# Kernel optimization log

Hardware: AMD Instinct MI355X
Metric: run time of the kernel (lower is better)

## Reference

```python
import jax, jax.numpy as jnp
import numpy as np

WH, WW = 7, 7
DIM, HEADS = 256, 8


def make_table_index(wh, ww):
    # relative coords table (log-spaced CPB input) and relative position index
    ch = np.arange(-(wh - 1), wh, dtype=np.float32)
    cw = np.arange(-(ww - 1), ww, dtype=np.float32)
    t = np.stack(np.meshgrid(ch, cw, indexing='ij'), axis=-1)[None]  # [1,2wh-1,2ww-1,2]
    t = t.copy()
    t[..., 0] /= (wh - 1)
    t[..., 1] /= (ww - 1)
    t *= 8.0
    t = np.sign(t) * np.log2(np.abs(t) + 1.0) / np.log2(8.0)
    coords = np.stack(np.meshgrid(np.arange(wh), np.arange(ww), indexing='ij'))
    cf = coords.reshape(2, -1)
    rc = (cf[:, :, None] - cf[:, None, :]).transpose(1, 2, 0).copy()  # [N,N,2]
    rc[..., 0] += wh - 1
    rc[..., 1] += ww - 1
    rc[..., 0] *= 2 * ww - 1
    idx = rc.sum(-1)
    return t.astype(np.float32), idx.astype(np.int32)


def setup_inputs() -> dict:
    key = jax.random.key(0)
    ks = jax.random.split(key, 10)
    B_, N, C, H = 2048, WH * WW, DIM, HEADS
    table, idx = make_table_index(WH, WW)
    return {
        'x': jax.random.normal(ks[0], (B_, N, C), jnp.float32),
        'mask': jnp.zeros((64, N, N), jnp.float32),
        'qkv_w': jax.random.normal(ks[1], (3 * C, C), jnp.float32) * 0.02,
        'q_bias': jnp.zeros((C,), jnp.float32),
        'v_bias': jnp.zeros((C,), jnp.float32),
        'logit_scale': jnp.full((H, 1, 1), np.log(10.0), jnp.float32),
        'cpb_w1': jax.random.normal(ks[2], (512, 2), jnp.float32) * 0.02,
        'cpb_b1': jnp.zeros((512,), jnp.float32),
        'cpb_w2': jax.random.normal(ks[3], (H, 512), jnp.float32) * 0.02,
        'proj_w': jax.random.normal(ks[4], (C, C), jnp.float32) * 0.02,
        'proj_b': jnp.zeros((C,), jnp.float32),
        'rel_coords_table': jnp.asarray(table),
        'rel_pos_index': jnp.asarray(idx),
    }


def _l2norm(t):
    return t / jnp.maximum(jnp.linalg.norm(t, axis=-1, keepdims=True), 1e-12)


def reference(x, mask, qkv_w, q_bias, v_bias, logit_scale, cpb_w1, cpb_b1,
              cpb_w2, proj_w, proj_b, rel_coords_table, rel_pos_index):
    B_, N, C = x.shape
    H = logit_scale.shape[0]
    hd = C // H
    qkv_b = jnp.concatenate([q_bias, jnp.zeros_like(v_bias), v_bias])
    qkv = (x @ qkv_w.T + qkv_b).reshape(B_, N, 3, H, hd).transpose(2, 0, 3, 1, 4)
    q, k, v = qkv[0], qkv[1], qkv[2]  # [B_,H,N,hd]
    attn = jnp.einsum('bhnd,bhmd->bhnm', _l2norm(q), _l2norm(k))
    scale = jnp.exp(jnp.minimum(logit_scale, jnp.log(jnp.float32(100.0))))  # [H,1,1]
    attn = attn * scale[None]
    # CPB MLP -> relative position bias
    table = jax.nn.relu(rel_coords_table @ cpb_w1.T + cpb_b1) @ cpb_w2.T  # [1,Th,Tw,H]
    table = table.reshape(-1, H)
    bias = table[rel_pos_index.reshape(-1)].reshape(N, N, H).transpose(2, 0, 1)
    attn = attn + 16.0 * jax.nn.sigmoid(bias)[None]
    nW = mask.shape[0]
    attn = attn.reshape(B_ // nW, nW, H, N, N) + mask[None, :, None]
    attn = jax.nn.softmax(attn.reshape(B_, H, N, N), axis=-1)
    out = jnp.einsum('bhnm,bhmd->bhnd', attn, v).transpose(0, 2, 1, 3).reshape(B_, N, C)
    return out @ proj_w.T + proj_b
```

## Files before the change

### kernel.cpp

```cpp
#include <hip/hip_runtime.h>

#define DEV __device__ __forceinline__

typedef float  f32x4  __attribute__((ext_vector_type(4)));
typedef __bf16 bf16x8 __attribute__((ext_vector_type(8)));

DEV unsigned short f2bf(float f) {
  unsigned u = __float_as_uint(f);
  u += 0x7fffu + ((u >> 16) & 1u);
  return (unsigned short)(u >> 16);
}
DEV float bf2f(unsigned short v) { return __uint_as_float(((unsigned)v) << 16); }

DEV void cp16(const void* g, void* l) {
  __builtin_amdgcn_global_load_lds((const __attribute__((address_space(1))) void*)g,
                                   (__attribute__((address_space(3))) void*)l, 16, 0, 0);
}

__global__ __launch_bounds__(256) void prep_kernel(
    const float* __restrict__ qkv_w, const float* __restrict__ proj_w,
    const float* __restrict__ q_bias, const float* __restrict__ v_bias,
    unsigned short* __restrict__ wq, unsigned short* __restrict__ wp,
    float* __restrict__ qkvb)
{
  int gid = blockIdx.x * 256 + threadIdx.x;
  if (gid < 196608) wq[gid] = f2bf(qkv_w[gid]);
  else              wp[gid - 196608] = f2bf(proj_w[gid - 196608]);
  if (gid < 768)
    qkvb[gid] = (gid < 256) ? q_bias[gid] : ((gid < 512) ? 0.f : v_bias[gid - 512]);
}

__global__ __launch_bounds__(256) void xcvt(const float* __restrict__ x,
                                            unsigned short* __restrict__ xb)
{
  const size_t g = ((size_t)blockIdx.x * 256 + threadIdx.x) * 8;
  float4 a = *(const float4*)(x + g);
  float4 b = *(const float4*)(x + g + 4);
  uint4 u;
  u.x = f2bf(a.x) | ((unsigned)f2bf(a.y) << 16);
  u.y = f2bf(a.z) | ((unsigned)f2bf(a.w) << 16);
  u.z = f2bf(b.x) | ((unsigned)f2bf(b.y) << 16);
  u.w = f2bf(b.z) | ((unsigned)f2bf(b.w) << 16);
  *(uint4*)(xb + g) = u;
}

__global__ __launch_bounds__(64) void cpb_mlp(
    const float* __restrict__ tab, const float* __restrict__ w1,
    const float* __restrict__ b1, const float* __restrict__ w2,
    float* __restrict__ table16)
{
  int r = blockIdx.x;
  int t = threadIdx.x;
  float x0 = tab[r * 2 + 0], x1 = tab[r * 2 + 1];
  float part[8];
#pragma unroll
  for (int h = 0; h < 8; ++h) part[h] = 0.f;
  for (int j = t; j < 512; j += 64) {
    float hv = fmaxf(w1[j * 2 + 0] * x0 + w1[j * 2 + 1] * x1 + b1[j], 0.f);
#pragma unroll
    for (int h = 0; h < 8; ++h) part[h] += hv * w2[h * 512 + j];
  }
#pragma unroll
  for (int h = 0; h < 8; ++h) {
    float v = part[h];
    for (int off = 32; off > 0; off >>= 1) v += __shfl_down(v, off, 64);
    if (t == 0) table16[r * 8 + h] = 16.f / (1.f + expf(-v));
  }
}

__global__ __launch_bounds__(256) void bmb(
    const float* __restrict__ t16, const int* __restrict__ ridx,
    const float* __restrict__ mask, float* __restrict__ bias64,
    float* __restrict__ mask64)
{
  int gid = blockIdx.x * 256 + threadIdx.x;
  int p = gid & 4095, i = p >> 6, j = p & 63;
  bool valid = (i < 49) && (j < 49);
  if (gid < 32768) {
    int h = gid >> 12;
    bias64[gid] = valid ? t16[ridx[i * 49 + j] * 8 + h] : 0.f;
  } else {
    int g2 = gid - 32768;
    int w = g2 >> 12;
    mask64[g2] = valid ? mask[w * 2401 + i * 49 + j] : 0.f;
  }
}

template <bool OBF16>
__global__ __launch_bounds__(256) void gemm128(
    const unsigned short* __restrict__ A, const unsigned short* __restrict__ W,
    const float* __restrict__ bias, void* __restrict__ Yp, int N, int K)
{
  __shared__ __align__(1024) unsigned short sA[128 * 64];
  __shared__ __align__(1024) unsigned short sB[128 * 64];
  const int t = threadIdx.x, w = t >> 6, l = t & 63, quad = l >> 4, l15 = l & 15;
  const int bm = blockIdx.y * 128, bn = blockIdx.x * 128;
  const int wm = (w >> 1) * 64, wn = (w & 1) * 64;
  const int srow = t >> 3, sch = t & 7;

  f32x4 acc[4][4] = {};
  const int KT = K >> 6;
  for (int kt = 0; kt < KT; ++kt) {
    const int k0 = kt << 6;
    if (kt) __syncthreads();
#pragma unroll
    for (int i = 0; i < 4; ++i) {
      const int row = i * 32 + srow;
      const int sc  = sch ^ (srow & 7);
      cp16(A + (size_t)(bm + row) * K + k0 + sc * 8, sA + (i * 256 + w * 64) * 8);
      cp16(W + (size_t)(bn + row) * K + k0 + sc * 8, sB + (i * 256 + w * 64) * 8);
    }
    __syncthreads();
#pragma unroll
    for (int kk = 0; kk < 2; ++kk) {
      bf16x8 af[4], bfr[4];
#pragma unroll
      for (int mt = 0; mt < 4; ++mt)
        af[mt] = *(const bf16x8*)&sA[(wm + mt * 16 + l15) * 64 + (((4 * kk + quad) ^ (l15 & 7)) * 8)];
#pragma unroll
      for (int nt = 0; nt < 4; ++nt)
        bfr[nt] = *(const bf16x8*)&sB[(wn + nt * 16 + l15) * 64 + (((4 * kk + quad) ^ (l15 & 7)) * 8)];
#pragma unroll
      for (int mt = 0; mt < 4; ++mt)
#pragma unroll
        for (int nt = 0; nt < 4; ++nt)
          acc[mt][nt] = __builtin_amdgcn_mfma_f32_16x16x32_bf16(af[mt], bfr[nt], acc[mt][nt], 0, 0, 0);
    }
  }
#pragma unroll
  for (int nt = 0; nt < 4; ++nt) {
    const int col = bn + wn + nt * 16 + l15;
    const float bv = bias[col];
#pragma unroll
    for (int mt = 0; mt < 4; ++mt) {
#pragma unroll
      for (int r = 0; r < 4; ++r) {
        const int row = bm + wm + mt * 16 + quad * 4 + r;
        float v = acc[mt][nt][r] + bv;
        if constexpr (OBF16) ((unsigned short*)Yp)[(size_t)row * N + col] = f2bf(v);
        else                 ((float*)Yp)[(size_t)row * N + col] = v;
      }
    }
  }
}

__global__ __launch_bounds__(256) void attn_mfma(
    const unsigned short* __restrict__ qkv, const float* __restrict__ logit_scale,
    const float* __restrict__ bias64, const float* __restrict__ mask64,
    unsigned short* __restrict__ aout)
{
  __shared__ __align__(1024) char smem[4 * 12800];
  const int w = threadIdx.x >> 6, l = threadIdx.x & 63, quad = l >> 4, l15 = l & 15;
  const int flat = blockIdx.x * 4 + w;
  const int b = flat >> 3, h = flat & 7;
  char* my = smem + w * 12800;
  unsigned short* vT = (unsigned short*)my;
  unsigned short* P  = (unsigned short*)(my + 4096);
  float* rq = (float*)(my + 12288);
  float* rk = (float*)(my + 12544);

  const size_t base = (size_t)b * 49 * 768 + h * 32;

  if (l < 49) {
    const unsigned short* qp = qkv + base + (size_t)l * 768;
    unsigned short qb_[32], kb_[32], vb_[32];
#pragma unroll
    for (int c = 0; c < 4; ++c) {
      *(uint4*)&qb_[c * 8] = *(const uint4*)(qp + c * 8);
      *(uint4*)&kb_[c * 8] = *(const uint4*)(qp + 256 + c * 8);
      *(uint4*)&vb_[c * 8] = *(const uint4*)(qp + 512 + c * 8);
    }
    float sq = 0.f, sk = 0.f;
#pragma unroll
    for (int d = 0; d < 32; ++d) {
      float qf = bf2f(qb_[d]), kf = bf2f(kb_[d]);
      sq += qf * qf; sk += kf * kf;
    }
    const float scale = __expf(fminf(logit_scale[h], 4.60517019f));
    rq[l] = scale / fmaxf(sqrtf(sq), 1e-12f);
    rk[l] = 1.f / fmaxf(sqrtf(sk), 1e-12f);
#pragma unroll
    for (int d = 0; d < 32; ++d)
      vT[d * 64 + (((l >> 3) ^ (d & 7)) << 3) + (l & 7)] = vb_[d];
  } else {
    rq[l] = 0.f; rk[l] = 0.f;
#pragma unroll
    for (int d = 0; d < 32; ++d)
      vT[d * 64 + (((l >> 3) ^ (d & 7)) << 3) + (l & 7)] = 0;
  }
  __syncthreads();

  f32x4 acc[4][4] = {};
  {
    const unsigned short* qb = qkv + base + quad * 8;
    const unsigned short* kb = qkv + base + 256 + quad * 8;
    bf16x8 kf[4], qf[4];
#pragma unroll
    for (int mt = 0; mt < 4; ++mt) kf[mt] = *(const bf16x8*)(kb + (size_t)(mt * 16 + l15) * 768);
#pragma unroll
    for (int nt = 0; nt < 4; ++nt) qf[nt] = *(const bf16x8*)(qb + (size_t)(nt * 16 + l15) * 768);
#pragma unroll
    for (int mt = 0; mt < 4; ++mt)
#pragma unroll
      for (int nt = 0; nt < 4; ++nt)
        acc[mt][nt] = __builtin_amdgcn_mfma_f32_16x16x32_bf16(kf[mt], qf[nt], acc[mt][nt], 0, 0, 0);
  }

  const float* bh = bias64 + (size_t)h * 4096;
  const float* mw = mask64 + (size_t)(b & 63) * 4096;
#pragma unroll
  for (int nt = 0; nt < 4; ++nt) {
    const int i = nt * 16 + l15;
    const float rqv = rq[i];
    float s[4][4];
    float mx = -1e30f;
#pragma unroll
    for (int mt = 0; mt < 4; ++mt) {
      const int jb = mt * 16 + quad * 4;
      const f32x4 b4  = *(const f32x4*)(bh + i * 64 + jb);
      const f32x4 m4  = *(const f32x4*)(mw + i * 64 + jb);
      const f32x4 rk4 = *(const f32x4*)(rk + jb);
#pragma unroll
      for (int r = 0; r < 4; ++r) {
        float sv = acc[mt][nt][r] * (rqv * rk4[r]) + b4[r] + m4[r];
        sv = (jb + r < 49) ? sv : -1e30f;
        s[mt][r] = sv;
        mx = fmaxf(mx, sv);
      }
    }
    mx = fmaxf(mx, __shfl_xor(mx, 16, 64));
    mx = fmaxf(mx, __shfl_xor(mx, 32, 64));
    float sum = 0.f;
    float p[4][4];
#pragma unroll
    for (int mt = 0; mt < 4; ++mt)
#pragma unroll
      for (int r = 0; r < 4; ++r) {
        float pv = __expf(s[mt][r] - mx);
        p[mt][r] = pv; sum += pv;
      }
    sum += __shfl_xor(sum, 16, 64);
    sum += __shfl_xor(sum, 32, 64);
    const float rs = 1.f / sum;
#pragma unroll
    for (int mt = 0; mt < 4; ++mt) {
      unsigned d0 = f2bf(p[mt][0] * rs) | ((unsigned)f2bf(p[mt][1] * rs) << 16);
      unsigned d1 = f2bf(p[mt][2] * rs) | ((unsigned)f2bf(p[mt][3] * rs) << 16);
      const int c = 2 * mt + (quad >> 1);
      uint2 uv; uv.x = d0; uv.y = d1;
      *(uint2*)((char*)P + i * 128 + ((c ^ (i & 7)) * 16) + (quad & 1) * 8) = uv;
    }
  }
  __syncthreads();

  f32x4 oacc[2][4] = {};
#pragma unroll
  for (int kk = 0; kk < 2; ++kk) {
    bf16x8 vf[2], pf[4];
#pragma unroll
    for (int mt = 0; mt < 2; ++mt)
      vf[mt] = *(const bf16x8*)((char*)vT + (mt * 16 + l15) * 128 + (((4 * kk + quad) ^ (l15 & 7)) * 16));
#pragma unroll
    for (int nt = 0; nt < 4; ++nt)
      pf[nt] = *(const bf16x8*)((char*)P + (nt * 16 + l15) * 128 + (((4 * kk + quad) ^ (l15 & 7)) * 16));
#pragma unroll
    for (int mt = 0; mt < 2; ++mt)
#pragma unroll
      for (int nt = 0; nt < 4; ++nt)
        oacc[mt][nt] = __builtin_amdgcn_mfma_f32_16x16x32_bf16(vf[mt], pf[nt], oacc[mt][nt], 0, 0, 0);
  }

#pragma unroll
  for (int nt = 0; nt < 4; ++nt) {
    const int tok = nt * 16 + l15;
    if (tok < 49) {
      unsigned short* op = aout + (size_t)(b * 49 + tok) * 256 + h * 32;
#pragma unroll
      for (int mt = 0; mt < 2; ++mt) {
        unsigned u0 = f2bf(oacc[mt][nt][0]) | ((unsigned)f2bf(oacc[mt][nt][1]) << 16);
        unsigned u1 = f2bf(oacc[mt][nt][2]) | ((unsigned)f2bf(oacc[mt][nt][3]) << 16);
        uint2 uv; uv.x = u0; uv.y = u1;
        *(uint2*)(op + mt * 16 + quad * 4) = uv;
      }
    }
  }
}

extern "C" void kernel_launch(void* const* d_in, const int* in_sizes, int n_in,
                              void* d_out, int out_size, void* d_ws, size_t ws_size,
                              hipStream_t stream) {
  const float* x           = (const float*)d_in[0];
  const float* mask        = (const float*)d_in[1];
  const float* qkv_w       = (const float*)d_in[2];
  const float* q_bias      = (const float*)d_in[3];
  const float* v_bias      = (const float*)d_in[4];
  const float* logit_scale = (const float*)d_in[5];
  const float* cpb_w1      = (const float*)d_in[6];
  const float* cpb_b1      = (const float*)d_in[7];
  const float* cpb_w2      = (const float*)d_in[8];
  const float* proj_w      = (const float*)d_in[9];
  const float* proj_b      = (const float*)d_in[10];
  const float* rel_tab     = (const float*)d_in[11];
  const int*   rel_idx     = (const int*)d_in[12];
  float*       out         = (float*)d_out;

  char* ws = (char*)d_ws;
  unsigned short* qkvws   = (unsigned short*)(ws + 0);
  unsigned short* shrd    = (unsigned short*)(ws + 154140672);
  unsigned short* wq      = (unsigned short*)(ws + 205520896);
  unsigned short* wp      = (unsigned short*)(ws + 205914112);
  float*          qkvb    = (float*)(ws + 206045184);
  float*          table16 = (float*)(ws + 206048256);
  float*          bias64  = (float*)(ws + 206053888);
  float*          mask64  = (float*)(ws + 206184960);

  prep_kernel<<<1024, 256, 0, stream>>>(qkv_w, proj_w, q_bias, v_bias, wq, wp, qkvb);
  cpb_mlp<<<169, 64, 0, stream>>>(rel_tab, cpb_w1, cpb_b1, cpb_w2, table16);
  xcvt<<<12544, 256, 0, stream>>>(x, shrd);
  gemm128<true><<<dim3(6, 784), 256, 0, stream>>>(shrd, wq, qkvb, qkvws, 768, 256);
  bmb<<<1152, 256, 0, stream>>>(table16, rel_idx, mask, bias64, mask64);
  attn_mfma<<<4096, 256, 0, stream>>>(qkvws, logit_scale, bias64, mask64, shrd);
  gemm128<false><<<dim3(2, 784), 256, 0, stream>>>(shrd, wp, proj_b, out, 256, 256);
}
```

Before: 430.1 us.

## Fuse x conversion into QKV GEMM and emit head-major QKV layout for attention

Removes the separate fp32-to-bf16 conversion pass over x by loading fp32 rows directly in the QKV GEMM and converting into LDS. The GEMM epilogue now scatters outputs into a per-(batch,head) contiguous q/k/v layout, so the attention kernel reads compact 49x32 tiles instead of strided 768-wide rows. Attention computes the q/k norms from MFMA fragments via shuffles, and the GEMM block order is remapped in groups of 8. The scattered 2-byte epilogue stores may coalesce worse than row-major stores.

```diff
diff --git a/kernel.cpp b/kernel.cpp
--- a/kernel.cpp
+++ b/kernel.cpp
@@ -28,20 +28,6 @@
   else              wp[gid - 196608] = f2bf(proj_w[gid - 196608]);
   if (gid < 768)
     qkvb[gid] = (gid < 256) ? q_bias[gid] : ((gid < 512) ? 0.f : v_bias[gid - 512]);
-}
-
-__global__ __launch_bounds__(256) void xcvt(const float* __restrict__ x,
-                                            unsigned short* __restrict__ xb)
-{
-  const size_t g = ((size_t)blockIdx.x * 256 + threadIdx.x) * 8;
-  float4 a = *(const float4*)(x + g);
-  float4 b = *(const float4*)(x + g + 4);
-  uint4 u;
-  u.x = f2bf(a.x) | ((unsigned)f2bf(a.y) << 16);
-  u.y = f2bf(a.z) | ((unsigned)f2bf(a.w) << 16);
-  u.z = f2bf(b.x) | ((unsigned)f2bf(b.y) << 16);
-  u.w = f2bf(b.z) | ((unsigned)f2bf(b.w) << 16);
-  *(uint4*)(xb + g) = u;
 }
 
 __global__ __launch_bounds__(64) void cpb_mlp(
@@ -86,6 +72,236 @@
   }
 }
 
+__global__ __launch_bounds__(256) void gemm_qkv(
+    const float* __restrict__ X, const unsigned short* __restrict__ W,
+    const float* __restrict__ bias, unsigned short* __restrict__ qkv)
+{
+  __shared__ __align__(1024) unsigned short sA[128 * 64];
+  __shared__ __align__(1024) unsigned short sB[128 * 64];
+  const int t = threadIdx.x, w = t >> 6, l = t & 63, quad = l >> 4, l15 = l & 15;
+  const int idx = blockIdx.x;
+  const int x8 = idx & 7, local = idx >> 3;
+  const int my = x8 * 98 + local / 6, bnb = local % 6;
+  const int bm = my * 128, bn = bnb * 128;
+  const int wm = (w >> 1) * 64, wn = (w & 1) * 64;
+  const int arow = t >> 1, ahalf = t & 1;
+  const int srow = t >> 3, sch = t & 7;
+
+  f32x4 acc[4][4] = {};
+#pragma unroll 1
+  for (int kt = 0; kt < 4; ++kt) {
+    const int k0 = kt << 6;
+    if (kt) __syncthreads();
+#pragma unroll
+    for (int i = 0; i < 4; ++i) {
+      const int row = i * 32 + srow;
+      const int sc  = sch ^ (srow & 7);
+      cp16(W + (size_t)(bn + row) * 256 + k0 + sc * 8, sB + (i * 256 + w * 64) * 8);
+    }
+    {
+      const float* ap = X + (size_t)(bm + arow) * 256 + k0 + ahalf * 32;
+#pragma unroll
+      for (int c = 0; c < 4; ++c) {
+        float4 f0 = *(const float4*)(ap + c * 8);
+        float4 f1 = *(const float4*)(ap + c * 8 + 4);
+        uint4 u;
+        u.x = f2bf(f0.x) | ((unsigned)f2bf(f0.y) << 16);
+        u.y = f2bf(f0.z) | ((unsigned)f2bf(f0.w) << 16);
+        u.z = f2bf(f1.x) | ((unsigned)f2bf(f1.y) << 16);
+        u.w = f2bf(f1.z) | ((unsigned)f2bf(f1.w) << 16);
+        const int cb = ahalf * 4 + c;
+        *(uint4*)&sA[arow * 64 + ((cb ^ (arow & 7)) * 8)] = u;
+      }
+    }
+    __syncthreads();
+#pragma unroll
+    for (int kk = 0; kk < 2; ++kk) {
+      bf16x8 af[4], bfr[4];
+#pragma unroll
+      for (int mt = 0; mt < 4; ++mt)
+        af[mt] = *(const bf16x8*)&sA[(wm + mt * 16 + l15) * 64 + (((4 * kk + quad) ^ (l15 & 7)) * 8)];
+#pragma unroll
+      for (int nt = 0; nt < 4; ++nt)
+        bfr[nt] = *(const bf16x8*)&sB[(wn + nt * 16 + l15) * 64 + (((4 * kk + quad) ^ (l15 & 7)) * 8)];
+#pragma unroll
+      for (int mt = 0; mt < 4; ++mt)
+#pragma unroll
+        for (int nt = 0; nt < 4; ++nt)
+          acc[mt][nt] = __builtin_amdgcn_mfma_f32_16x16x32_bf16(af[mt], bfr[nt], acc[mt][nt], 0, 0, 0);
+    }
+  }
+  unsigned bq[16]; int tq[16];
+#pragma unroll
+  for (int mt = 0; mt < 4; ++mt)
+#pragma unroll
+    for (int r = 0; r < 4; ++r) {
+      const int row = bm + wm + mt * 16 + quad * 4 + r;
+      const unsigned bb = (unsigned)(((unsigned long long)row * 87652394ull) >> 32);
+      bq[mt * 4 + r] = bb;
+      tq[mt * 4 + r] = row - (int)bb * 49;
+    }
+#pragma unroll
+  for (int nt = 0; nt < 4; ++nt) {
+    const int col0 = bn + wn + nt * 16;
+    const int s = col0 >> 8, h = (col0 >> 5) & 7, dbase = col0 & 31;
+    const int d = dbase + l15;
+    const float bv = bias[col0 + l15];
+#pragma unroll
+    for (int mt = 0; mt < 4; ++mt)
+#pragma unroll
+      for (int r = 0; r < 4; ++r) {
+        const unsigned bb = bq[mt * 4 + r];
+        const int tok = tq[mt * 4 + r];
+        qkv[(size_t)((bb * 8u + h) * 3u + s) * 1568 + tok * 32 + d] =
+            f2bf(acc[mt][nt][r] + bv);
+      }
+  }
+}
+
+__global__ __launch_bounds__(256) void attn2(
+    const unsigned short* __restrict__ qkv, const float* __restrict__ logit_scale,
+    const float* __restrict__ bias64, const float* __restrict__ mask64,
+    unsigned short* __restrict__ aout)
+{
+  __shared__ __align__(1024) char smem[4 * 12544];
+  const int w = threadIdx.x >> 6, l = threadIdx.x & 63, quad = l >> 4, l15 = l & 15;
+  const int flat = blockIdx.x * 4 + w;
+  const int b = flat >> 3, h = flat & 7;
+  char* my = smem + w * 12544;
+  unsigned short* vT = (unsigned short*)my;
+  unsigned short* P  = (unsigned short*)(my + 4096);
+  float* rk = (float*)(my + 12288);
+
+  const unsigned short* qb = qkv + (size_t)flat * 4704;
+  const unsigned short* kb = qb + 1568;
+  const unsigned short* vb = qb + 3136;
+
+  bf16x8 kf[4], qf[4];
+#pragma unroll
+  for (int mt = 0; mt < 4; ++mt) kf[mt] = *(const bf16x8*)(kb + (mt * 16 + l15) * 32 + quad * 8);
+#pragma unroll
+  for (int nt = 0; nt < 4; ++nt) qf[nt] = *(const bf16x8*)(qb + (nt * 16 + l15) * 32 + quad * 8);
+
+  const float scale = __expf(fminf(logit_scale[h], 4.60517019f));
+  float rqv[4];
+#pragma unroll
+  for (int nt = 0; nt < 4; ++nt) {
+    float s = 0.f;
+#pragma unroll
+    for (int d = 0; d < 8; ++d) { float f = (float)qf[nt][d]; s += f * f; }
+    s += __shfl_xor(s, 16, 64); s += __shfl_xor(s, 32, 64);
+    rqv[nt] = scale / fmaxf(sqrtf(s), 1e-12f);
+  }
+#pragma unroll
+  for (int mt = 0; mt < 4; ++mt) {
+    float s = 0.f;
+#pragma unroll
+    for (int d = 0; d < 8; ++d) { float f = (float)kf[mt][d]; s += f * f; }
+    s += __shfl_xor(s, 16, 64); s += __shfl_xor(s, 32, 64);
+    if (quad == 0) rk[mt * 16 + l15] = 1.f / fmaxf(sqrtf(s), 1e-12f);
+  }
+
+  if (l < 49) {
+    unsigned short vv[32];
+#pragma unroll
+    for (int c = 0; c < 4; ++c) *(uint4*)&vv[c * 8] = *(const uint4*)(vb + l * 32 + c * 8);
+#pragma unroll
+    for (int d = 0; d < 32; ++d)
+      vT[d * 64 + (((l >> 3) ^ (d & 7)) << 3) + (l & 7)] = vv[d];
+  } else {
+#pragma unroll
+    for (int d = 0; d < 32; ++d)
+      vT[d * 64 + (((l >> 3) ^ (d & 7)) << 3) + (l & 7)] = 0;
+  }
+  __syncthreads();
+
+  f32x4 acc[4][4] = {};
+#pragma unroll
+  for (int mt = 0; mt < 4; ++mt)
+#pragma unroll
+    for (int nt = 0; nt < 4; ++nt)
+      acc[mt][nt] = __builtin_amdgcn_mfma_f32_16x16x32_bf16(kf[mt], qf[nt], acc[mt][nt], 0, 0, 0);
+
+  const float* bh = bias64 + (size_t)h * 4096;
+  const float* mw = mask64 + (size_t)(b & 63) * 4096;
+#pragma unroll
+  for (int nt = 0; nt < 4; ++nt) {
+    const int i = nt * 16 + l15;
+    const float rqi = rqv[nt];
+    float s[4][4];
+    float mx = -1e30f;
+#pragma unroll
+    for (int mt = 0; mt < 4; ++mt) {
+      const int jb = mt * 16 + quad * 4;
+      const f32x4 b4  = *(const f32x4*)(bh + i * 64 + jb);
+      const f32x4 m4  = *(const f32x4*)(mw + i * 64 + jb);
+      const f32x4 rk4 = *(const f32x4*)(rk + jb);
+#pragma unroll
+      for (int r = 0; r < 4; ++r) {
+        float sv = acc[mt][nt][r] * (rqi * rk4[r]) + b4[r] + m4[r];
+        sv = (jb + r < 49) ? sv : -1e30f;
+        s[mt][r] = sv;
+        mx = fmaxf(mx, sv);
+      }
+    }
+    mx = fmaxf(mx, __shfl_xor(mx, 16, 64));
+    mx = fmaxf(mx, __shfl_xor(mx, 32, 64));
+    float sum = 0.f;
+    float p[4][4];
+#pragma unroll
+    for (int mt = 0; mt < 4; ++mt)
+#pragma unroll
+      for (int r = 0; r < 4; ++r) {
+        float pv = __expf(s[mt][r] - mx);
+        p[mt][r] = pv; sum += pv;
+      }
+    sum += __shfl_xor(sum, 16, 64);
+    sum += __shfl_xor(sum, 32, 64);
+    const float rs = 1.f / sum;
+#pragma unroll
+    for (int mt = 0; mt < 4; ++mt) {
+      unsigned d0 = f2bf(p[mt][0] * rs) | ((unsigned)f2bf(p[mt][1] * rs) << 16);
+      unsigned d1 = f2bf(p[mt][2] * rs) | ((unsigned)f2bf(p[mt][3] * rs) << 16);
+      const int c = 2 * mt + (quad >> 1);
+      uint2 uv; uv.x = d0; uv.y = d1;
+      *(uint2*)((char*)P + i * 128 + ((c ^ (i & 7)) * 16) + (quad & 1) * 8) = uv;
+    }
+  }
+  __syncthreads();
+
+  f32x4 oacc[2][4] = {};
+#pragma unroll
+  for (int kk = 0; kk < 2; ++kk) {
+    bf16x8 vf[2], pf[4];
+#pragma unroll
+    for (int mt = 0; mt < 2; ++mt)
+      vf[mt] = *(const bf16x8*)((char*)vT + (mt * 16 + l15) * 128 + (((4 * kk + quad) ^ (l15 & 7)) * 16));
+#pragma unroll
+    for (int nt = 0; nt < 4; ++nt)
+      pf[nt] = *(const bf16x8*)((char*)P + (nt * 16 + l15) * 128 + (((4 * kk + quad) ^ (l15 & 7)) * 16));
+#pragma unroll
+    for (int mt = 0; mt < 2; ++mt)
+#pragma unroll
+      for (int nt = 0; nt < 4; ++nt)
+        oacc[mt][nt] = __builtin_amdgcn_mfma_f32_16x16x32_bf16(vf[mt], pf[nt], oacc[mt][nt], 0, 0, 0);
+  }
+
+#pragma unroll
+  for (int nt = 0; nt < 4; ++nt) {
+    const int tok = nt * 16 + l15;
+    if (tok < 49) {
+      unsigned short* op = aout + (size_t)(b * 49 + tok) * 256 + h * 32;
+#pragma unroll
+      for (int mt = 0; mt < 2; ++mt) {
+        unsigned u0 = f2bf(oacc[mt][nt][0]) | ((unsigned)f2bf(oacc[mt][nt][1]) << 16);
+        unsigned u1 = f2bf(oacc[mt][nt][2]) | ((unsigned)f2bf(oacc[mt][nt][3]) << 16);
+        uint2 uv; uv.x = u0; uv.y = u1;
+        *(uint2*)(op + mt * 16 + quad * 4) = uv;
+      }
+    }
+  }
+}
+
 template <bool OBF16>
 __global__ __launch_bounds__(256) void gemm128(
     const unsigned short* __restrict__ A, const unsigned short* __restrict__ W,
@@ -139,148 +355,6 @@
         float v = acc[mt][nt][r] + bv;
         if constexpr (OBF16) ((unsigned short*)Yp)[(size_t)row * N + col] = f2bf(v);
         else                 ((float*)Yp)[(size_t)row * N + col] = v;
-      }
-    }
-  }
-}
-
-__global__ __launch_bounds__(256) void attn_mfma(
-    const unsigned short* __restrict__ qkv, const float* __restrict__ logit_scale,
-    const float* __restrict__ bias64, const float* __restrict__ mask64,
-    unsigned short* __restrict__ aout)
-{
-  __shared__ __align__(1024) char smem[4 * 12800];
-  const int w = threadIdx.x >> 6, l = threadIdx.x & 63, quad = l >> 4, l15 = l & 15;
-  const int flat = blockIdx.x * 4 + w;
-  const int b = flat >> 3, h = flat & 7;
-  char* my = smem + w * 12800;
-  unsigned short* vT = (unsigned short*)my;
-  unsigned short* P  = (unsigned short*)(my + 4096);
-  float* rq = (float*)(my + 12288);
-  float* rk = (float*)(my + 12544);
-
-  const size_t base = (size_t)b * 49 * 768 + h * 32;
-
-  if (l < 49) {
-    const unsigned short* qp = qkv + base + (size_t)l * 768;
-    unsigned short qb_[32], kb_[32], vb_[32];
-#pragma unroll
-    for (int c = 0; c < 4; ++c) {
-      *(uint4*)&qb_[c * 8] = *(const uint4*)(qp + c * 8);
-      *(uint4*)&kb_[c * 8] = *(const uint4*)(qp + 256 + c * 8);
-      *(uint4*)&vb_[c * 8] = *(const uint4*)(qp + 512 + c * 8);
-    }
-    float sq = 0.f, sk = 0.f;
-#pragma unroll
-    for (int d = 0; d < 32; ++d) {
-      float qf = bf2f(qb_[d]), kf = bf2f(kb_[d]);
-      sq += qf * qf; sk += kf * kf;
-    }
-    const float scale = __expf(fminf(logit_scale[h], 4.60517019f));
-    rq[l] = scale / fmaxf(sqrtf(sq), 1e-12f);
-    rk[l] = 1.f / fmaxf(sqrtf(sk), 1e-12f);
-#pragma unroll
-    for (int d = 0; d < 32; ++d)
-      vT[d * 64 + (((l >> 3) ^ (d & 7)) << 3) + (l & 7)] = vb_[d];
-  } else {
-    rq[l] = 0.f; rk[l] = 0.f;
-#pragma unroll
-    for (int d = 0; d < 32; ++d)
-      vT[d * 64 + (((l >> 3) ^ (d & 7)) << 3) + (l & 7)] = 0;
-  }
-  __syncthreads();
-
-  f32x4 acc[4][4] = {};
-  {
-    const unsigned short* qb = qkv + base + quad * 8;
-    const unsigned short* kb = qkv + base + 256 + quad * 8;
-    bf16x8 kf[4], qf[4];
-#pragma unroll
-    for (int mt = 0; mt < 4; ++mt) kf[mt] = *(const bf16x8*)(kb + (size_t)(mt * 16 + l15) * 768);
-#pragma unroll
-    for (int nt = 0; nt < 4; ++nt) qf[nt] = *(const bf16x8*)(qb + (size_t)(nt * 16 + l15) * 768);
-#pragma unroll
-    for (int mt = 0; mt < 4; ++mt)
-#pragma unroll
-      for (int nt = 0; nt < 4; ++nt)
-        acc[mt][nt] = __builtin_amdgcn_mfma_f32_16x16x32_bf16(kf[mt], qf[nt], acc[mt][nt], 0, 0, 0);
-  }
-
-  const float* bh = bias64 + (size_t)h * 4096;
-  const float* mw = mask64 + (size_t)(b & 63) * 4096;
-#pragma unroll
-  for (int nt = 0; nt < 4; ++nt) {
-    const int i = nt * 16 + l15;
-    const float rqv = rq[i];
-    float s[4][4];
-    float mx = -1e30f;
-#pragma unroll
-    for (int mt = 0; mt < 4; ++mt) {
-      const int jb = mt * 16 + quad * 4;
-      const f32x4 b4  = *(const f32x4*)(bh + i * 64 + jb);
-      const f32x4 m4  = *(const f32x4*)(mw + i * 64 + jb);
-      const f32x4 rk4 = *(const f32x4*)(rk + jb);
-#pragma unroll
-      for (int r = 0; r < 4; ++r) {
-        float sv = acc[mt][nt][r] * (rqv * rk4[r]) + b4[r] + m4[r];
-        sv = (jb + r < 49) ? sv : -1e30f;
-        s[mt][r] = sv;
-        mx = fmaxf(mx, sv);
-      }
-    }
-    mx = fmaxf(mx, __shfl_xor(mx, 16, 64));
-    mx = fmaxf(mx, __shfl_xor(mx, 32, 64));
-    float sum = 0.f;
-    float p[4][4];
-#pragma unroll
-    for (int mt = 0; mt < 4; ++mt)
-#pragma unroll
-      for (int r = 0; r < 4; ++r) {
-        float pv = __expf(s[mt][r] - mx);
-        p[mt][r] = pv; sum += pv;
-      }
-    sum += __shfl_xor(sum, 16, 64);
-    sum += __shfl_xor(sum, 32, 64);
-    const float rs = 1.f / sum;
-#pragma unroll
-    for (int mt = 0; mt < 4; ++mt) {
-      unsigned d0 = f2bf(p[mt][0] * rs) | ((unsigned)f2bf(p[mt][1] * rs) << 16);
-      unsigned d1 = f2bf(p[mt][2] * rs) | ((unsigned)f2bf(p[mt][3] * rs) << 16);
-      const int c = 2 * mt + (quad >> 1);
-      uint2 uv; uv.x = d0; uv.y = d1;
-      *(uint2*)((char*)P + i * 128 + ((c ^ (i & 7)) * 16) + (quad & 1) * 8) = uv;
-    }
-  }
-  __syncthreads();
-
-  f32x4 oacc[2][4] = {};
-#pragma unroll
-  for (int kk = 0; kk < 2; ++kk) {
-    bf16x8 vf[2], pf[4];
-#pragma unroll
-    for (int mt = 0; mt < 2; ++mt)
-      vf[mt] = *(const bf16x8*)((char*)vT + (mt * 16 + l15) * 128 + (((4 * kk + quad) ^ (l15 & 7)) * 16));
-#pragma unroll
-    for (int nt = 0; nt < 4; ++nt)
-      pf[nt] = *(const bf16x8*)((char*)P + (nt * 16 + l15) * 128 + (((4 * kk + quad) ^ (l15 & 7)) * 16));
-#pragma unroll
-    for (int mt = 0; mt < 2; ++mt)
-#pragma unroll
-      for (int nt = 0; nt < 4; ++nt)
-        oacc[mt][nt] = __builtin_amdgcn_mfma_f32_16x16x32_bf16(vf[mt], pf[nt], oacc[mt][nt], 0, 0, 0);
-  }
-
-#pragma unroll
-  for (int nt = 0; nt < 4; ++nt) {
-    const int tok = nt * 16 + l15;
-    if (tok < 49) {
-      unsigned short* op = aout + (size_t)(b * 49 + tok) * 256 + h * 32;
-#pragma unroll
-      for (int mt = 0; mt < 2; ++mt) {
-        unsigned u0 = f2bf(oacc[mt][nt][0]) | ((unsigned)f2bf(oacc[mt][nt][1]) << 16);
-        unsigned u1 = f2bf(oacc[mt][nt][2]) | ((unsigned)f2bf(oacc[mt][nt][3]) << 16);
-        uint2 uv; uv.x = u0; uv.y = u1;
-        *(uint2*)(op + mt * 16 + quad * 4) = uv;
       }
     }
   }
@@ -305,8 +379,8 @@
   float*       out         = (float*)d_out;
 
   char* ws = (char*)d_ws;
-  unsigned short* qkvws   = (unsigned short*)(ws + 0);
-  unsigned short* shrd    = (unsigned short*)(ws + 154140672);
+  unsigned short* qkvp    = (unsigned short*)(ws + 0);
+  unsigned short* aows    = (unsigned short*)(ws + 154140672);
   unsigned short* wq      = (unsigned short*)(ws + 205520896);
   unsigned short* wp      = (unsigned short*)(ws + 205914112);
   float*          qkvb    = (float*)(ws + 206045184);
@@ -316,9 +390,8 @@
 
   prep_kernel<<<1024, 256, 0, stream>>>(qkv_w, proj_w, q_bias, v_bias, wq, wp, qkvb);
   cpb_mlp<<<169, 64, 0, stream>>>(rel_tab, cpb_w1, cpb_b1, cpb_w2, table16);
-  xcvt<<<12544, 256, 0, stream>>>(x, shrd);
-  gemm128<true><<<dim3(6, 784), 256, 0, stream>>>(shrd, wq, qkvb, qkvws, 768, 256);
   bmb<<<1152, 256, 0, stream>>>(table16, rel_idx, mask, bias64, mask64);
-  attn_mfma<<<4096, 256, 0, stream>>>(qkvws, logit_scale, bias64, mask64, shrd);
-  gemm128<false><<<dim3(2, 784), 256, 0, stream>>>(shrd, wp, proj_b, out, 256, 256);
-}
+  gemm_qkv<<<4704, 256, 0, stream>>>(x, wq, qkvb, qkvp);
+  attn2<<<4096, 256, 0, stream>>>(qkvp, logit_scale, bias64, mask64, aows);
+  gemm128<false><<<dim3(2, 784), 256, 0, stream>>>(aows, wp, proj_b, out, 256, 256);
+}
```

Result: slower. 441.6 us (+2.7%).
